# Kernel optimization log

Hardware: AMD Instinct MI355X
Metric: run time of the kernel (lower is better)

## Reference

```python
import jax, jax.numpy as jnp
import numpy as np

SEQ, BATCH, HIDDEN = 2048, 2, 1024
NUM_HEADS, HEAD_DIM = 16, 64
LN_EPS = 1e-6
NEG_INF = -1e10


def setup_inputs() -> dict:
    key = jax.random.key(0)
    k1, k2, k3, k4 = jax.random.split(key, 4)
    inputs_q = jax.random.normal(k1, (SEQ, BATCH, HIDDEN), dtype=jnp.float32)
    # mask convention (TE flax): True / 1 => position is masked out
    mask = jax.random.randint(k2, (BATCH, 1, SEQ, SEQ), 0, 2).astype(bool)
    ln_scale = jnp.ones((HIDDEN,), dtype=jnp.float32)
    ln_bias = jnp.zeros((HIDDEN,), dtype=jnp.float32)
    # fused QKV kernel (embed, 3, num_heads*head_dim); query column pre-scaled
    # at init by 1/sqrt(head_dim) (scaled_query_init=True)
    w_qkv = jax.random.normal(k3, (HIDDEN, 3, NUM_HEADS * HEAD_DIM), dtype=jnp.float32) / np.sqrt(HIDDEN)
    w_qkv = w_qkv.at[:, 0, :].divide(np.sqrt(HEAD_DIM))
    w_out = jax.random.normal(k4, (NUM_HEADS * HEAD_DIM, HIDDEN), dtype=jnp.float32) / np.sqrt(NUM_HEADS * HEAD_DIM)
    return {"inputs_q": inputs_q, "mask": mask, "ln_scale": ln_scale,
            "ln_bias": ln_bias, "w_qkv": w_qkv, "w_out": w_out}


def _layernorm(x, scale, bias):
    mean = jnp.mean(x, axis=-1, keepdims=True)
    var = jnp.mean(jnp.square(x - mean), axis=-1, keepdims=True)
    return (x - mean) * jax.lax.rsqrt(var + LN_EPS) * scale + bias


def reference(inputs_q, mask, ln_scale, ln_bias, w_qkv, w_out):
    s, b, e = inputs_q.shape  # (seq, batch, hidden): transpose_batch_sequence=True
    ln_out = _layernorm(inputs_q, ln_scale, ln_bias)
    # fused QKV projection: (s,b,e) @ (e,3,H*D) -> (s,b,3,H*D)
    qkv = jnp.einsum('sbe,ekf->sbkf', ln_out, w_qkv)
    q, k, v = qkv[:, :, 0, :], qkv[:, :, 1, :], qkv[:, :, 2, :]
    q = q.reshape(s, b, NUM_HEADS, HEAD_DIM)
    k = k.reshape(s, b, NUM_HEADS, HEAD_DIM)
    v = v.reshape(s, b, NUM_HEADS, HEAD_DIM)
    # core attention, transpose_batch_sequence layout (seq, batch, h, d)
    logits = jnp.einsum('qbhd,kbhd->bhqk', q, k)
    logits = jnp.where(mask, jnp.asarray(NEG_INF, logits.dtype), logits)
    attn = jax.nn.softmax(logits, axis=-1)
    ctx = jnp.einsum('bhqk,kbhd->qbhd', attn, v).reshape(s, b, NUM_HEADS * HEAD_DIM)
    out = jnp.einsum('sbf,fe->sbe', ctx, w_out)
    return out
```

## Files before the change

kernel.cpp:

```cpp
#include <hip/hip_runtime.h>

typedef __bf16 bf16;
typedef __attribute__((ext_vector_type(8))) __bf16 bf16x8;
typedef __attribute__((ext_vector_type(4))) __bf16 bf16x4;
typedef __attribute__((ext_vector_type(4))) float f32x4;
typedef unsigned long long u64;

static constexpr int S = 2048, B = 2, H = 1024, NH = 16, HD = 64;
static constexpr int ROWS = S * B;
static constexpr int NQKV = 3 * NH * HD;
static constexpr int KBLK = 64;
static constexpr int NT = S / KBLK;
static constexpr int MW = S / 64;
static constexpr float LOG2E = 1.4426950408889634f;

__device__ __forceinline__ int swz(int row, int col) { return col ^ ((row & 7) << 3); }

__device__ __forceinline__ void g2l16(const bf16* g, bf16* l) {
  __builtin_amdgcn_global_load_lds((const __attribute__((address_space(1))) void*)g,
                                   (__attribute__((address_space(3))) void*)l, 16, 0, 0);
}

__global__ __launch_bounds__(256) void prep_kernel(const float* __restrict__ wqkv,
                                                   const float* __restrict__ wout,
                                                   bf16* __restrict__ dqkv,
                                                   bf16* __restrict__ dout,
                                                   const float* __restrict__ x,
                                                   const float* __restrict__ sc,
                                                   const float* __restrict__ bi,
                                                   bf16* __restrict__ lnout,
                                                   const unsigned char* __restrict__ mbytes,
                                                   int* __restrict__ flag) {
  __shared__ float shmem[32 * 33];
  const int bid = blockIdx.x;
  const int tid = threadIdx.x;
  if (bid < 4096) {
    const int bx = bid & 127, by = bid >> 7;
    const bool second = bx >= (NQKV / 32);
    const float* src = second ? wout : wqkv;
    bf16* dst = second ? dout : dqkv;
    const int C = second ? H : NQKV;
    const int c0 = (second ? bx - NQKV / 32 : bx) * 32, r0 = by * 32;
    const int xx = tid & 31, yy = tid >> 5;
#pragma unroll
    for (int i = 0; i < 32; i += 8)
      shmem[(yy + i) * 33 + xx] = src[(size_t)(r0 + yy + i) * C + c0 + xx];
    __syncthreads();
#pragma unroll
    for (int i = 0; i < 32; i += 8) {
      const int col = c0 + yy + i;
      const float scale = (!second && col < 1024) ? LOG2E : 1.0f;
      dst[(size_t)col * H + r0 + xx] = (bf16)(shmem[xx * 33 + yy + i] * scale);
    }
  } else if (bid < 8192) {
    const int row = bid - 4096;
    const float4 v = *(const float4*)&x[(size_t)row * H + tid * 4];
    float s = v.x + v.y + v.z + v.w;
#pragma unroll
    for (int m = 1; m < 64; m <<= 1) s += __shfl_xor(s, m);
    float* red1 = shmem;
    float* red2 = shmem + 8;
    const int w = tid >> 6, lane = tid & 63;
    if (lane == 0) red1[w] = s;
    __syncthreads();
    const float mean = (red1[0] + red1[1] + red1[2] + red1[3]) * (1.0f / H);
    const float dx = v.x - mean, dy = v.y - mean, dz = v.z - mean, dw = v.w - mean;
    float q = dx * dx + dy * dy + dz * dz + dw * dw;
#pragma unroll
    for (int m = 1; m < 64; m <<= 1) q += __shfl_xor(q, m);
    if (lane == 0) red2[w] = q;
    __syncthreads();
    const float var = (red2[0] + red2[1] + red2[2] + red2[3]) * (1.0f / H);
    const float inv = rsqrtf(var + 1e-6f);
    const float4 s4 = *(const float4*)&sc[tid * 4];
    const float4 b4 = *(const float4*)&bi[tid * 4];
    bf16x4 o;
    o[0] = (bf16)(dx * inv * s4.x + b4.x);
    o[1] = (bf16)(dy * inv * s4.y + b4.y);
    o[2] = (bf16)(dz * inv * s4.z + b4.z);
    o[3] = (bf16)(dw * inv * s4.w + b4.w);
    *(bf16x4*)&lnout[(size_t)row * H + tid * 4] = o;
  } else {
    int* cnt = (int*)shmem;
    if (tid == 0) cnt[0] = 0;
    __syncthreads();
    int local = 0;
    for (int i = tid; i < 4096; i += 256)
      if ((i & 3) != 0 && mbytes[i] != 0) local = 1;
    if (local) atomicOr(cnt, 1);
    __syncthreads();
    if (tid == 0) flag[0] = (cnt[0] == 0) ? 1 : 0;
  }
}

__global__ __launch_bounds__(256) void pack_mask(const void* __restrict__ mask, const int* __restrict__ flag,
                                                 u64* __restrict__ bits) {
  const size_t e = (size_t)blockIdx.x * 256 + threadIdx.x;
  int mv;
  if (flag[0] != 0) mv = ((const int*)mask)[e];
  else mv = (int)((const unsigned char*)mask)[e];
  const u64 bal = __ballot(mv != 0);
  if ((threadIdx.x & 63) == 0) bits[e >> 6] = bal;
}

template <int EPI>
__global__ __launch_bounds__(256) void gemm128(const bf16* __restrict__ A, const bf16* __restrict__ Bt,
                                               bf16* __restrict__ qo, bf16* __restrict__ ko,
                                               bf16* __restrict__ vo, float* __restrict__ out) {
  constexpr int K = 1024;
  constexpr int NKT = K / 64;
  __shared__ __align__(16) bf16 As[2][128][64];
  __shared__ __align__(16) bf16 Bs[2][128][64];
  const int nwg = gridDim.x * gridDim.y;
  const int lin = blockIdx.y * gridDim.x + blockIdx.x;
  const int cpx = nwg >> 3;
  const int work = (lin & 7) * cpx + (lin >> 3);
  const int bm = (work / gridDim.x) * 128, bn = (work % gridDim.x) * 128;
  const int tid = threadIdx.x;
  const int wave = tid >> 6, lane = tid & 63;
  const int wm = (wave >> 1) * 64, wn = (wave & 1) * 64;
  const int g = lane >> 4, l15 = lane & 15;
  const int lr = lane >> 3;
  const int lc = 8 * ((lane & 7) ^ lr);
  const bf16* Ab = &A[(size_t)bm * K];
  const bf16* Bb = &Bt[(size_t)bn * K];

  f32x4 acc[4][4] = {};
#pragma unroll
  for (int p = 0; p < 4; ++p) {
    const int r0 = wave * 32 + p * 8;
    g2l16(&Ab[(size_t)(r0 + lr) * K + lc], &As[0][r0][0]);
    g2l16(&Bb[(size_t)(r0 + lr) * K + lc], &Bs[0][r0][0]);
  }
  __syncthreads();

  for (int kt = 0; kt < NKT; ++kt) {
    const int cur = kt & 1;
    if (kt + 1 < NKT) {
      const int ko2 = (kt + 1) * 64;
#pragma unroll
      for (int p = 0; p < 4; ++p) {
        const int r0 = wave * 32 + p * 8;
        g2l16(&Ab[(size_t)(r0 + lr) * K + ko2 + lc], &As[cur ^ 1][r0][0]);
        g2l16(&Bb[(size_t)(r0 + lr) * K + ko2 + lc], &Bs[cur ^ 1][r0][0]);
      }
    }
#pragma unroll
    for (int ks = 0; ks < 2; ++ks) {
      bf16x8 af[4], bb[4];
#pragma unroll
      for (int i = 0; i < 4; ++i) af[i] = *(const bf16x8*)&As[cur][wm + i * 16 + l15][swz(l15, ks * 32 + g * 8)];
#pragma unroll
      for (int j = 0; j < 4; ++j) bb[j] = *(const bf16x8*)&Bs[cur][wn + j * 16 + l15][swz(l15, ks * 32 + g * 8)];
      __builtin_amdgcn_s_setprio(1);
#pragma unroll
      for (int i = 0; i < 4; ++i)
#pragma unroll
        for (int j = 0; j < 4; ++j)
          acc[i][j] = __builtin_amdgcn_mfma_f32_16x16x32_bf16(af[i], bb[j], acc[i][j], 0, 0, 0);
      __builtin_amdgcn_s_setprio(0);
    }
    __syncthreads();
  }
#pragma unroll
  for (int i = 0; i < 4; ++i) {
#pragma unroll
    for (int j = 0; j < 4; ++j) {
#pragma unroll
      for (int r = 0; r < 4; ++r) {
        const int row = bm + wm + i * 16 + g * 4 + r;
        const int col = bn + wn + j * 16 + l15;
        const float val = acc[i][j][r];
        if (EPI == 0) {
          const int kk = col >> 10, f = col & 1023;
          const int h = f >> 6, d = f & 63;
          const int sdx = row >> 1, b = row & 1;
          const size_t head = (size_t)b * NH + h;
          if (kk == 0)
            qo[(head * S + sdx) * HD + d] = (bf16)val;
          else if (kk == 1)
            ko[(head * S + sdx) * HD + d] = (bf16)val;
          else
            vo[(head * HD + d) * S + sdx] = (bf16)val;
        } else {
          out[(size_t)row * H + col] = val;
        }
      }
    }
  }
}

__global__ __launch_bounds__(512, 4) void attn_kernel(const bf16* __restrict__ Qb, const bf16* __restrict__ Kb,
                                                      const bf16* __restrict__ Vt, const u64* __restrict__ mbits,
                                                      bf16* __restrict__ ctx) {
  __shared__ __align__(16) bf16 Ks[2][64][64];
  __shared__ __align__(16) bf16 Vs[2][64][64];
  __shared__ __align__(16) bf16 P[8][16][64];
  const int lin = blockIdx.y * 16 + blockIdx.x;
  const int work = ((lin & 7) << 6) | (lin >> 3);
  const int bh = work >> 4, qb = work & 15;
  const int b = bh >> 4, h = bh & 15;
  const int tid = threadIdx.x, w = tid >> 6, lane = tid & 63;
  const int g = lane >> 4, c = lane & 15;
  const int q0 = qb * 128 + w * 16;
  const size_t head = (size_t)b * NH + h;
  const bf16* Qh = Qb + head * S * HD;
  const bf16* Kh = Kb + head * S * HD;
  const bf16* Vh = Vt + head * HD * S;

  const int srow = w * 8 + (lane >> 3);
  const int scol = 8 * ((lane & 7) ^ (lane >> 3));

  bf16x8 aq[2];
#pragma unroll
  for (int ks = 0; ks < 2; ++ks)
    aq[ks] = *(const bf16x8*)&Qh[(size_t)(q0 + c) * HD + ks * 32 + g * 8];

  f32x4 o[4] = {};
  float lsum = 0.f;

  g2l16(&Kh[(size_t)srow * HD + scol], &Ks[0][w * 8][0]);
  g2l16(&Vh[(size_t)srow * S + scol], &Vs[0][w * 8][0]);
  __syncthreads();

  for (int t = 0; t < NT; ++t) {
    const int cur = t & 1;
    if (t + 1 < NT) {
      const int kt1 = (t + 1) * KBLK;
      g2l16(&Kh[(size_t)(kt1 + srow) * HD + scol], &Ks[cur ^ 1][w * 8][0]);
      g2l16(&Vh[(size_t)srow * S + kt1 + scol], &Vs[cur ^ 1][w * 8][0]);
    }
    f32x4 sv[4] = {};
#pragma unroll
    for (int ks = 0; ks < 2; ++ks) {
      bf16x8 bk[4];
#pragma unroll
      for (int j = 0; j < 4; ++j)
        bk[j] = *(const bf16x8*)&Ks[cur][j * 16 + c][swz(c, ks * 32 + g * 8)];
      __builtin_amdgcn_s_setprio(1);
#pragma unroll
      for (int j = 0; j < 4; ++j)
        sv[j] = __builtin_amdgcn_mfma_f32_16x16x32_bf16(bk[j], aq[ks], sv[j], 0, 0, 0);
      __builtin_amdgcn_s_setprio(0);
    }
    {
      const u64 mb = mbits[((size_t)b * S + q0 + c) * MW + t];
      const unsigned mlo = (unsigned)mb, mhi = (unsigned)(mb >> 32);
      f32x4 acc4 = {0.f, 0.f, 0.f, 0.f};
#pragma unroll
      for (int j = 0; j < 4; ++j) {
        const unsigned word = (j < 2) ? mlo : mhi;
        const unsigned sub = word >> (((j & 1) << 4) + (g << 2));
        bf16x4 pk;
#pragma unroll
        for (int r = 0; r < 4; ++r) {
          float e = __builtin_amdgcn_exp2f(sv[j][r]);
          if ((sub >> r) & 1u) e = 0.f;
          pk[r] = (bf16)e;
          acc4[r] += e;
        }
        *(bf16x4*)&P[w][c][(j * 16 + g * 4) ^ ((c & 7) << 3)] = pk;
      }
      float part = (acc4[0] + acc4[1]) + (acc4[2] + acc4[3]);
      part += __shfl_xor(part, 16);
      part += __shfl_xor(part, 32);
      lsum += part;
    }
    __threadfence_block();
#pragma unroll
    for (int ks = 0; ks < 2; ++ks) {
      const bf16x8 pa = *(const bf16x8*)&P[w][c][(ks * 32 + g * 8) ^ ((c & 7) << 3)];
      bf16x8 bv[4];
#pragma unroll
      for (int j = 0; j < 4; ++j)
        bv[j] = *(const bf16x8*)&Vs[cur][j * 16 + c][swz(c, ks * 32 + g * 8)];
      __builtin_amdgcn_s_setprio(1);
#pragma unroll
      for (int j = 0; j < 4; ++j)
        o[j] = __builtin_amdgcn_mfma_f32_16x16x32_bf16(pa, bv[j], o[j], 0, 0, 0);
      __builtin_amdgcn_s_setprio(0);
    }
    __syncthreads();
  }
#pragma unroll
  for (int r = 0; r < 4; ++r) {
    const float denom = __shfl(lsum, g * 4 + r);
    const float inv = 1.0f / denom;
    const int qrow = q0 + g * 4 + r;
#pragma unroll
    for (int j = 0; j < 4; ++j)
      ctx[((size_t)qrow * B + b) * H + h * HD + j * 16 + c] = (bf16)(o[j][r] * inv);
  }
}

extern "C" void kernel_launch(void* const* d_in, const int* in_sizes, int n_in,
                              void* d_out, int out_size, void* d_ws, size_t ws_size,
                              hipStream_t stream) {
  const float* x = (const float*)d_in[0];
  const void* mask = d_in[1];
  const float* ln_scale = (const float*)d_in[2];
  const float* ln_bias = (const float*)d_in[3];
  const float* w_qkv = (const float*)d_in[4];
  const float* w_out = (const float*)d_in[5];
  float* out = (float*)d_out;

  char* ws = (char*)d_ws;
  size_t off = 0;
  int* flag = (int*)(ws + off); off += 256;
  u64* mbits = (u64*)(ws + off); off += (size_t)B * S * (S / 8);
  bf16* lnb   = (bf16*)(ws + off); off += (size_t)ROWS * H * 2;
  bf16* wqkvt = (bf16*)(ws + off); off += (size_t)NQKV * H * 2;
  bf16* woutt = (bf16*)(ws + off); off += (size_t)H * H * 2;
  bf16* Qb    = (bf16*)(ws + off); off += (size_t)B * NH * S * HD * 2;
  bf16* Kb    = (bf16*)(ws + off); off += (size_t)B * NH * S * HD * 2;
  bf16* Vt    = (bf16*)(ws + off); off += (size_t)B * NH * S * HD * 2;
  bf16* ctx   = (bf16*)(ws + off); off += (size_t)ROWS * H * 2;

  prep_kernel<<<8193, 256, 0, stream>>>(w_qkv, w_out, wqkvt, woutt, x, ln_scale, ln_bias, lnb,
                                        (const unsigned char*)mask, flag);
  pack_mask<<<(B * S * S) / 256, 256, 0, stream>>>(mask, flag, mbits);
  gemm128<0><<<dim3(NQKV / 128, ROWS / 128), 256, 0, stream>>>(lnb, wqkvt, Qb, Kb, Vt, nullptr);
  attn_kernel<<<dim3(S / 128, B * NH), 512, 0, stream>>>(Qb, Kb, Vt, mbits, ctx);
  gemm128<1><<<dim3(H / 128, ROWS / 128), 256, 0, stream>>>(ctx, woutt, nullptr, nullptr, nullptr, out);
}
```

Baseline: 161.1 us.

## Fold mask packing into QKV GEMM launch and transpose V tile epilogue

Removes the standalone pack_mask kernel by appending extra workgroups to the QKV GEMM grid that pack the mask bits, with each packing workgroup handling 16 chunks. This saves one launch and lets the packing overlap with the GEMM tiles. Separately, for V tiles the MFMA operands are swapped so each lane holds consecutive d values along rows. The intent is to make the transposed V store less scattered. The cost is extra branching in the GEMM and a 1D grid remap.

```diff
diff --git a/kernel.cpp b/kernel.cpp
--- a/kernel.cpp
+++ b/kernel.cpp
@@ -13,6 +13,8 @@
 static constexpr int NT = S / KBLK;
 static constexpr int MW = S / 64;
 static constexpr float LOG2E = 1.4426950408889634f;
+static constexpr int G0_WG = (NQKV / 128) * (ROWS / 128);
+static constexpr int PACK_WG = (B * S * S) / (256 * 16);
 
 __device__ __forceinline__ int swz(int row, int col) { return col ^ ((row & 7) << 3); }
 
@@ -93,29 +95,43 @@
   }
 }
 
-__global__ __launch_bounds__(256) void pack_mask(const void* __restrict__ mask, const int* __restrict__ flag,
-                                                 u64* __restrict__ bits) {
-  const size_t e = (size_t)blockIdx.x * 256 + threadIdx.x;
-  int mv;
-  if (flag[0] != 0) mv = ((const int*)mask)[e];
-  else mv = (int)((const unsigned char*)mask)[e];
-  const u64 bal = __ballot(mv != 0);
-  if ((threadIdx.x & 63) == 0) bits[e >> 6] = bal;
-}
-
 template <int EPI>
 __global__ __launch_bounds__(256) void gemm128(const bf16* __restrict__ A, const bf16* __restrict__ Bt,
                                                bf16* __restrict__ qo, bf16* __restrict__ ko,
-                                               bf16* __restrict__ vo, float* __restrict__ out) {
+                                               bf16* __restrict__ vo, float* __restrict__ out,
+                                               const void* __restrict__ mask, const int* __restrict__ flag,
+                                               u64* __restrict__ bits) {
   constexpr int K = 1024;
   constexpr int NKT = K / 64;
   __shared__ __align__(16) bf16 As[2][128][64];
   __shared__ __align__(16) bf16 Bs[2][128][64];
-  const int nwg = gridDim.x * gridDim.y;
-  const int lin = blockIdx.y * gridDim.x + blockIdx.x;
-  const int cpx = nwg >> 3;
+  int lin, NX, total;
+  if (EPI == 0) {
+    lin = blockIdx.x;
+    if (lin >= G0_WG) {
+      const size_t base = (size_t)(lin - G0_WG) * 4096;
+      const bool imode = (flag[0] != 0);
+      const int tid = threadIdx.x;
+#pragma unroll
+      for (int k = 0; k < 16; ++k) {
+        const size_t e = base + k * 256 + tid;
+        int mv;
+        if (imode) mv = ((const int*)mask)[e];
+        else mv = (int)((const unsigned char*)mask)[e];
+        const u64 bal = __ballot(mv != 0);
+        if ((tid & 63) == 0) bits[e >> 6] = bal;
+      }
+      return;
+    }
+    NX = NQKV / 128; total = G0_WG;
+  } else {
+    lin = blockIdx.y * gridDim.x + blockIdx.x;
+    NX = gridDim.x; total = gridDim.x * gridDim.y;
+  }
+  const int cpx = total >> 3;
   const int work = (lin & 7) * cpx + (lin >> 3);
-  const int bm = (work / gridDim.x) * 128, bn = (work % gridDim.x) * 128;
+  const int bm = (work / NX) * 128, bn = (work % NX) * 128;
+  const bool isV = (EPI == 0) && (bn >= 2048);
   const int tid = threadIdx.x;
   const int wave = tid >> 6, lane = tid & 63;
   const int wm = (wave >> 1) * 64, wn = (wave & 1) * 64;
@@ -153,11 +169,19 @@
 #pragma unroll
       for (int j = 0; j < 4; ++j) bb[j] = *(const bf16x8*)&Bs[cur][wn + j * 16 + l15][swz(l15, ks * 32 + g * 8)];
       __builtin_amdgcn_s_setprio(1);
-#pragma unroll
-      for (int i = 0; i < 4; ++i)
-#pragma unroll
-        for (int j = 0; j < 4; ++j)
-          acc[i][j] = __builtin_amdgcn_mfma_f32_16x16x32_bf16(af[i], bb[j], acc[i][j], 0, 0, 0);
+      if (isV) {
+#pragma unroll
+        for (int i = 0; i < 4; ++i)
+#pragma unroll
+          for (int j = 0; j < 4; ++j)
+            acc[i][j] = __builtin_amdgcn_mfma_f32_16x16x32_bf16(bb[j], af[i], acc[i][j], 0, 0, 0);
+      } else {
+#pragma unroll
+        for (int i = 0; i < 4; ++i)
+#pragma unroll
+          for (int j = 0; j < 4; ++j)
+            acc[i][j] = __builtin_amdgcn_mfma_f32_16x16x32_bf16(af[i], bb[j], acc[i][j], 0, 0, 0);
+      }
       __builtin_amdgcn_s_setprio(0);
     }
     __syncthreads();
@@ -168,21 +192,28 @@
     for (int j = 0; j < 4; ++j) {
 #pragma unroll
       for (int r = 0; r < 4; ++r) {
-        const int row = bm + wm + i * 16 + g * 4 + r;
-        const int col = bn + wn + j * 16 + l15;
         const float val = acc[i][j][r];
-        if (EPI == 0) {
+        if (isV) {
+          const int row = bm + wm + i * 16 + l15;
+          const int col = bn + wn + j * 16 + g * 4 + r;
+          const int f = col & 1023;
+          const int h = f >> 6, d = f & 63;
+          const int sdx = row >> 1, b = row & 1;
+          vo[(((size_t)b * NH + h) * HD + d) * S + sdx] = (bf16)val;
+        } else if (EPI == 0) {
+          const int row = bm + wm + i * 16 + g * 4 + r;
+          const int col = bn + wn + j * 16 + l15;
           const int kk = col >> 10, f = col & 1023;
           const int h = f >> 6, d = f & 63;
           const int sdx = row >> 1, b = row & 1;
           const size_t head = (size_t)b * NH + h;
           if (kk == 0)
             qo[(head * S + sdx) * HD + d] = (bf16)val;
-          else if (kk == 1)
+          else
             ko[(head * S + sdx) * HD + d] = (bf16)val;
-          else
-            vo[(head * HD + d) * S + sdx] = (bf16)val;
         } else {
+          const int row = bm + wm + i * 16 + g * 4 + r;
+          const int col = bn + wn + j * 16 + l15;
           out[(size_t)row * H + col] = val;
         }
       }
@@ -318,8 +349,8 @@
 
   prep_kernel<<<8193, 256, 0, stream>>>(w_qkv, w_out, wqkvt, woutt, x, ln_scale, ln_bias, lnb,
                                         (const unsigned char*)mask, flag);
-  pack_mask<<<(B * S * S) / 256, 256, 0, stream>>>(mask, flag, mbits);
-  gemm128<0><<<dim3(NQKV / 128, ROWS / 128), 256, 0, stream>>>(lnb, wqkvt, Qb, Kb, Vt, nullptr);
+  gemm128<0><<<G0_WG + PACK_WG, 256, 0, stream>>>(lnb, wqkvt, Qb, Kb, Vt, nullptr, mask, flag, mbits);
   attn_kernel<<<dim3(S / 128, B * NH), 512, 0, stream>>>(Qb, Kb, Vt, mbits, ctx);
-  gemm128<1><<<dim3(H / 128, ROWS / 128), 256, 0, stream>>>(ctx, woutt, nullptr, nullptr, nullptr, out);
-}
+  gemm128<1><<<dim3(H / 128, ROWS / 128), 256, 0, stream>>>(ctx, woutt, nullptr, nullptr, nullptr, out,
+                                                            nullptr, nullptr, nullptr);
+}
```

Result: faster. 151.5 us (-6.0%).
